# Optimization experiments

Measured on AMD Instinct MI355X. Metric: run time of the kernel, lower is better.

## Reference

```python
import jax, jax.numpy as jnp
import numpy as np

B, NQ, NKV, QD, KVD, AD = 8, 4096, 4096, 1024, 1024, 128

def setup_inputs() -> dict:
    key = jax.random.key(0)
    ks = jax.random.split(key, 6)
    scale = lambda d: 1.0 / np.sqrt(d)
    return {
        "q": jax.random.normal(ks[0], (B, NQ, QD), dtype=jnp.float32),
        "k": jax.random.normal(ks[1], (B, NKV, KVD), dtype=jnp.float32),
        "v": jax.random.normal(ks[2], (B, NKV, KVD), dtype=jnp.float32),
        "Wq": jax.random.normal(ks[3], (QD, AD), dtype=jnp.float32) * scale(QD),
        "Wk": jax.random.normal(ks[4], (KVD, AD), dtype=jnp.float32) * scale(KVD),
        "Wv": jax.random.normal(ks[5], (KVD, AD), dtype=jnp.float32) * scale(KVD),
    }

def reference(q, k, v, Wq, Wk, Wv):
    s = AD ** (-0.5)
    Q = jnp.einsum('bnd,de->bne', q, Wq)   # [B,NQ,AD]
    K = jnp.einsum('bmd,de->bme', k, Wk)   # [B,NKV,AD]
    V = jnp.einsum('bmd,de->bme', v, Wv)   # [B,NKV,AD]
    sc = jnp.einsum('bne,bme->bnm', Q, K) * s  # [B,NQ,NKV]
    att = jax.nn.softmax(sc, axis=-1)
    return jnp.einsum('bnm,bme->bne', att, V)
```

## Files before the change

kernel.cpp:

```cpp
#include <hip/hip_runtime.h>
#include <cstdint>
#include <cstddef>

typedef __bf16 bf16_t;
typedef __bf16 bf16x8 __attribute__((ext_vector_type(8)));
typedef __bf16 bf16x4v __attribute__((ext_vector_type(4)));
typedef float f32x16 __attribute__((ext_vector_type(16)));

static __device__ __forceinline__ f32x16 mfma32(bf16x8 a, bf16x8 b, f32x16 c) {
  return __builtin_amdgcn_mfma_f32_32x32x16_bf16(a, b, c, 0, 0, 0);
}

static __device__ __forceinline__ void gld_lds16(const void* g, void* l) {
  __builtin_amdgcn_global_load_lds(
      (const __attribute__((address_space(1))) unsigned int*)g,
      (__attribute__((address_space(3))) unsigned int*)l, 16, 0, 0);
}

#define CEXP_CONST 0.12754582f


__global__ void wt_kernel(const float* __restrict__ Wq, const float* __restrict__ Wk,
                          const float* __restrict__ Wv, bf16_t* __restrict__ Wt2) {
  int t = blockIdx.x * 256 + threadIdx.x;
  int tensor = t >> 17;
  int r = t & 131071;
  int j = r & 7, l31 = (r >> 3) & 31, h = (r >> 8) & 1, nf = (r >> 9) & 3, k16 = (r >> 11) & 63;
  int k = k16 * 16 + h * 8 + j, n = nf * 32 + l31;
  const float* W = tensor == 0 ? Wq : (tensor == 1 ? Wk : Wv);
  Wt2[t] = (bf16_t)W[(size_t)k * 128 + n];
}

__global__ __launch_bounds__(256, 4) void proj_kernel(
    const float* __restrict__ xq, const float* __restrict__ xk, const float* __restrict__ xv,
    const bf16_t* __restrict__ WtAll,
    bf16_t* __restrict__ Qp, bf16_t* __restrict__ Kp, bf16_t* __restrict__ Vt) {
  __shared__ __align__(16) char smc[16384];
  const int tid = threadIdx.x;
  const int ty = blockIdx.y;
  const int bm = blockIdx.x;
  const float* X = (ty == 0) ? xq : (ty == 1) ? xk : xv;
  const bf16_t* W2 = WtAll + (size_t)ty * 131072;
  const int lane = tid & 63;
  const int w = tid >> 6;
  const int l31 = lane & 31, h = lane >> 5;

  const char* aG = (const char*)X + (size_t)bm * 131072;

  float4 S[4];
  auto ldg = [&](int p) {
#pragma unroll
    for (int i = 0; i < 4; ++i) {
      int c = i * 256 + tid;
      S[i] = *(const float4*)(aG + (size_t)(c >> 5) * 4096 + p * 512 + (c & 31) * 16);
    }
  };
  auto stg = [&](int buf) {
#pragma unroll
    for (int i = 0; i < 4; ++i) {
      int c = i * 256 + tid;
      int row = c >> 5, s = c & 31;
      bf16x4v bv;
      bv[0] = (bf16_t)S[i].x; bv[1] = (bf16_t)S[i].y;
      bv[2] = (bf16_t)S[i].z; bv[3] = (bf16_t)S[i].w;
      int dst = buf * 8192 + row * 256 + ((((s >> 1) ^ (row & 7)) << 4)) + (s & 1) * 8;
      *(uint2*)(smc + dst) = __builtin_bit_cast(uint2, bv);
    }
  };

  bf16x8 wA[8], wB[8];
  const bf16_t* wbase = W2 + w * 512 + lane * 8;
  auto ldw = [&](bf16x8 (&Wf)[8], int p) {
#pragma unroll
    for (int kk = 0; kk < 8; ++kk)
      Wf[kk] = *(const bf16x8*)(wbase + (size_t)(p * 8 + kk) * 2048);
  };

  f32x16 acc;
#pragma unroll
  for (int r = 0; r < 16; ++r) acc[r] = 0.0f;
  const int asw = l31 & 7;
  auto kloop = [&](bf16x8 (&Wf)[8], int buf) {
    const char* arow = smc + buf * 8192 + l31 * 256;
#pragma unroll
    for (int kk = 0; kk < 8; ++kk) {
      bf16x8 af = *(const bf16x8*)(arow + (((kk * 2 + h) ^ asw) << 4));
      acc = mfma32(af, Wf[kk], acc);
    }
  };

  ldg(0);
  stg(0);
  ldg(1);
  ldw(wA, 0);
  __syncthreads();

#pragma unroll
  for (int p2 = 0; p2 < 4; ++p2) {
    const int pe = 2 * p2;
    ldw(wB, pe + 1);
    kloop(wA, 0);
    stg(1);
    if (pe + 2 < 8) ldg(pe + 2);
    __syncthreads();
    const int po = pe + 1;
    if (po + 1 < 8) ldw(wA, po + 1);
    kloop(wB, 1);
    if (po + 1 < 8) {
      stg(0);
      if (po + 2 < 8) ldg(po + 2);
    }
    __syncthreads();
  }

  if (ty < 2) {
    constexpr int RS = 264;
#pragma unroll
    for (int r = 0; r < 16; ++r) {
      int m = (r & 3) + 8 * (r >> 2) + 4 * h;
      *(bf16_t*)(smc + m * RS + (w * 32 + l31) * 2) = (bf16_t)acc[r];
    }
    __syncthreads();
    bf16_t* O = (ty == 0) ? Qp : Kp;
    char* obase = (char*)O + (size_t)bm * 8192;
#pragma unroll
    for (int i = 0; i < 2; ++i) {
      int c = i * 256 + tid;
      int rr = c >> 4, ch = c & 15;
      uint4 vv = *(const uint4*)(smc + rr * RS + ch * 16);
      *(uint4*)(obase + rr * 256 + ch * 16) = vv;
    }
  } else {
#pragma unroll
    for (int q = 0; q < 4; ++q) {
      int n = w * 32 + l31;
      bf16x4v bv;
#pragma unroll
      for (int j = 0; j < 4; ++j) bv[j] = (bf16_t)acc[q * 4 + j];
      *(uint2*)(smc + n * 72 + q * 16 + h * 8) = __builtin_bit_cast(uint2, bv);
    }
    __syncthreads();
    const int bb = bm >> 7;
    const int m0 = (bm & 127) * 32;
    {
      int n = tid >> 1, half = tid & 1;
      const char* src = smc + n * 72 + half * 32;
      char* dst = (char*)Vt + (size_t)bb * 1048576 + (size_t)n * 8192 + m0 * 2 + half * 32;
      uint4 v0 = *(const uint4*)(src);
      uint4 v1 = *(const uint4*)(src + 16);
      *(uint4*)(dst) = v0;
      *(uint4*)(dst + 16) = v1;
    }
  }
}

template <int B0>
static __device__ __forceinline__ bf16x8 build_pf(const f32x16& s, int h) {
  unsigned c0, c1, c2, c3;
  asm("v_cvt_pk_bf16_f32 %0, %1, %2" : "=v"(c0) : "v"(s[B0 + 0]), "v"(s[B0 + 1]));
  asm("v_cvt_pk_bf16_f32 %0, %1, %2" : "=v"(c1) : "v"(s[B0 + 2]), "v"(s[B0 + 3]));
  asm("v_cvt_pk_bf16_f32 %0, %1, %2" : "=v"(c2) : "v"(s[B0 + 4]), "v"(s[B0 + 5]));
  asm("v_cvt_pk_bf16_f32 %0, %1, %2" : "=v"(c3) : "v"(s[B0 + 6]), "v"(s[B0 + 7]));
  unsigned x0 = (unsigned)__shfl_xor((int)c0, 32);
  unsigned x1 = (unsigned)__shfl_xor((int)c1, 32);
  unsigned x2 = (unsigned)__shfl_xor((int)c2, 32);
  unsigned x3 = (unsigned)__shfl_xor((int)c3, 32);
  uint4 u;
  u.x = h ? x2 : c0;
  u.y = h ? x3 : c1;
  u.z = h ? c2 : x0;
  u.w = h ? c3 : x1;
  return __builtin_bit_cast(bf16x8, u);
}

template <int SPLIT>
__global__ __launch_bounds__(256, 2) void attn_kernel(
    const bf16_t* __restrict__ Qp, const bf16_t* __restrict__ Kp,
    const bf16_t* __restrict__ Vt, float* __restrict__ out,
    float* __restrict__ Opart, float* __restrict__ Mpart, float* __restrict__ Lpart) {
  __shared__ __align__(16) char smc[65536];
  const int tid = threadIdx.x;
  const int lane = tid & 63, w = tid >> 6;
  const int l31 = lane & 31, h = lane >> 5;
  const int bid = blockIdx.x;
  const int b = bid & 7;
  const int qt = (bid >> 3) & 31;
  const int s = bid >> 8;
  const int NT = 64 / SPLIT;
  const float CEXP = CEXP_CONST;
  const int qbase = qt * 128 + w * 32;
  const int sw0 = (l31 ^ (l31 >> 3)) & 7;
  const int sw1 = sw0 ^ 4;

  bf16x8 qf[8];
  const bf16_t* qrow = Qp + (size_t)(b * 4096 + qbase + l31) * 128 + h * 8;
#pragma unroll
  for (int db = 0; db < 8; ++db) qf[db] = *(const bf16x8*)(qrow + db * 16);

  int swv[4];
#pragma unroll
  for (int nf = 0; nf < 4; ++nf) swv[nf] = (l31 & 7) ^ ((4 * nf + (l31 >> 3)) & 7);

  const int rl = lane >> 4, slK = lane & 15;
  const int dl = lane >> 3, slV = lane & 7;
  int koff[4], voff[4];
#pragma unroll
  for (int i = 0; i < 4; ++i) {
    int r = w * 16 + i * 4 + rl;
    int swr = (r ^ (r >> 3)) & 7;
    koff[i] = r * 256 + (((slK & 8) | ((slK & 7) ^ swr)) << 4);
    int d = w * 32 + i * 8 + dl;
    int swd = (d ^ (d >> 3)) & 7;
    voff[i] = d * 8192 + ((slV ^ swd) << 4);
  }
  const char* kpb = (const char*)Kp + (size_t)b * 1048576 + (size_t)s * NT * 16384;
  const char* vpb = (const char*)Vt + (size_t)b * 1048576 + (size_t)s * NT * 128;

  f32x16 oacc[4];
#pragma unroll
  for (int nf = 0; nf < 4; ++nf)
#pragma unroll
    for (int r = 0; r < 16; ++r) oacc[nf][r] = 0.0f;
  float m_run = -3.0e38f, lacc = 0.0f;

  auto stage = [&](int tt, int bufb) {
    const char* kb = kpb + (size_t)tt * 16384;
    const char* vb = vpb + (size_t)tt * 128;
    char* lk = smc + bufb + w * 4096;
    char* lv = smc + bufb + 16384 + w * 4096;
#pragma unroll
    for (int i = 0; i < 4; ++i) {
      gld_lds16(kb + koff[i], lk + i * 1024);
      gld_lds16(vb + voff[i], lv + i * 1024);
    }
  };

  stage(0, 0);
  stage(1, 32768);

  for (int t = 0; t < NT; ++t) {
    asm volatile("s_waitcnt vmcnt(8)" ::: "memory");
    __builtin_amdgcn_s_barrier();
    const char* kb = smc + (t & 1) * 32768;
    const char* vb = kb + 16384;

    f32x16 s0, s1;
#pragma unroll
    for (int i = 0; i < 16; ++i) { s0[i] = 0.0f; s1[i] = 0.0f; }
    __builtin_amdgcn_s_setprio(1);
#pragma unroll
    for (int db = 0; db < 8; ++db) {
      const int q = 2 * db + h;
      bf16x8 k0 = *(const bf16x8*)(kb + l31 * 256 + (((q & 8) | ((q & 7) ^ sw0)) << 4));
      bf16x8 k1 = *(const bf16x8*)(kb + (32 + l31) * 256 + (((q & 8) | ((q & 7) ^ sw1)) << 4));
      s0 = mfma32(k0, qf[db], s0);
      s1 = mfma32(k1, qf[db], s1);
    }
    __builtin_amdgcn_s_setprio(0);

    float tmax = fmaxf(s0[0], s1[0]);
#pragma unroll
    for (int i = 1; i < 16; ++i) tmax = fmaxf(tmax, fmaxf(s0[i], s1[i]));
    tmax = fmaxf(tmax, __shfl_xor(tmax, 32));
    if (__any(tmax > m_run + 62.0f)) {
      float mnew = fmaxf(m_run, tmax);
      float fac = exp2f((m_run - mnew) * CEXP);
      m_run = mnew;
      lacc *= fac;
#pragma unroll
      for (int r = 0; r < 16; ++r) {
        float fr = __shfl(fac, (r & 3) + 8 * (r >> 2) + 4 * h);
#pragma unroll
        for (int nf = 0; nf < 4; ++nf) oacc[nf][r] *= fr;
      }
    }
    const float mc = m_run * CEXP;
#pragma unroll
    for (int i = 0; i < 16; ++i) s0[i] = exp2f(fmaf(s0[i], CEXP, -mc));
#pragma unroll
    for (int i = 0; i < 16; ++i) s1[i] = exp2f(fmaf(s1[i], CEXP, -mc));
    float a0 = 0.f, a1 = 0.f, a2 = 0.f, a3 = 0.f;
#pragma unroll
    for (int i = 0; i < 16; i += 4) {
      a0 += s0[i] + s1[i];         a1 += s0[i + 1] + s1[i + 1];
      a2 += s0[i + 2] + s1[i + 2]; a3 += s0[i + 3] + s1[i + 3];
    }
    lacc += (a0 + a1) + (a2 + a3);

    __builtin_amdgcn_s_setprio(1);
    {
      bf16x8 pf = build_pf<0>(s0, h);
#pragma unroll
      for (int nf = 0; nf < 4; ++nf) {
        bf16x8 vf = *(const bf16x8*)(vb + (nf * 32 + l31) * 128 + (((0 + h) ^ swv[nf]) << 4));
        oacc[nf] = mfma32(pf, vf, oacc[nf]);
      }
    }
    {
      bf16x8 pf = build_pf<8>(s0, h);
#pragma unroll
      for (int nf = 0; nf < 4; ++nf) {
        bf16x8 vf = *(const bf16x8*)(vb + (nf * 32 + l31) * 128 + (((2 + h) ^ swv[nf]) << 4));
        oacc[nf] = mfma32(pf, vf, oacc[nf]);
      }
    }
    {
      bf16x8 pf = build_pf<0>(s1, h);
#pragma unroll
      for (int nf = 0; nf < 4; ++nf) {
        bf16x8 vf = *(const bf16x8*)(vb + (nf * 32 + l31) * 128 + (((4 + h) ^ swv[nf]) << 4));
        oacc[nf] = mfma32(pf, vf, oacc[nf]);
      }
    }
    {
      bf16x8 pf = build_pf<8>(s1, h);
#pragma unroll
      for (int nf = 0; nf < 4; ++nf) {
        bf16x8 vf = *(const bf16x8*)(vb + (nf * 32 + l31) * 128 + (((6 + h) ^ swv[nf]) << 4));
        oacc[nf] = mfma32(pf, vf, oacc[nf]);
      }
    }
    __builtin_amdgcn_s_setprio(0);

    __builtin_amdgcn_s_barrier();
    stage((t + 2) & (NT - 1), (t & 1) * 32768);
  }
  asm volatile("s_waitcnt vmcnt(0)" ::: "memory");

  lacc += __shfl_xor(lacc, 32);
  if (SPLIT == 1) {
    const float inv = 1.0f / lacc;
    float* ob = out + (size_t)(b * 4096 + qbase) * 128;
#pragma unroll
    for (int r = 0; r < 16; ++r) {
      const int rowD = (r & 3) + 8 * (r >> 2) + 4 * h;
      float ir = __shfl(inv, rowD);
#pragma unroll
      for (int nf = 0; nf < 4; ++nf)
        ob[(size_t)rowD * 128 + nf * 32 + l31] = oacc[nf][r] * ir;
    }
  } else {
    const int pb = s * 256 + b * 32 + qt;
    if (lane < 32) {
      Mpart[pb * 128 + w * 32 + l31] = m_run;
      Lpart[pb * 128 + w * 32 + l31] = lacc;
    }
    float* ob = Opart + ((size_t)pb * 128 + w * 32) * 128;
#pragma unroll
    for (int r = 0; r < 16; ++r) {
      const int rowD = (r & 3) + 8 * (r >> 2) + 4 * h;
#pragma unroll
      for (int nf = 0; nf < 4; ++nf)
        ob[(size_t)rowD * 128 + nf * 32 + l31] = oacc[nf][r];
    }
  }
}

__global__ __launch_bounds__(256) void combine_kernel(
    const float* __restrict__ Opart, const float* __restrict__ Mpart,
    const float* __restrict__ Lpart, float* __restrict__ out) {
  const int g = blockIdx.x * 8 + (threadIdx.x >> 5);
  const int lane32 = threadIdx.x & 31;
  const int b = g >> 12;
  const int pos = g & 4095;
  const int qt = pos >> 7;
  const int row = pos & 127;
  const int i0 = (b * 32 + qt) * 128 + row;
  const int i1 = (256 + b * 32 + qt) * 128 + row;
  const float m0 = Mpart[i0], m1 = Mpart[i1];
  const float l0 = Lpart[i0], l1 = Lpart[i1];
  const float m = fmaxf(m0, m1);
  const float w0 = exp2f((m0 - m) * CEXP_CONST);
  const float w1 = exp2f((m1 - m) * CEXP_CONST);
  const float inv = 1.0f / (w0 * l0 + w1 * l1);
  const float4 o0 = *(const float4*)(Opart + (size_t)i0 * 128 + lane32 * 4);
  const float4 o1 = *(const float4*)(Opart + (size_t)i1 * 128 + lane32 * 4);
  float4 o;
  o.x = (w0 * o0.x + w1 * o1.x) * inv;
  o.y = (w0 * o0.y + w1 * o1.y) * inv;
  o.z = (w0 * o0.z + w1 * o1.z) * inv;
  o.w = (w0 * o0.w + w1 * o1.w) * inv;
  *(float4*)(out + (size_t)g * 128 + lane32 * 4) = o;
}

extern "C" void kernel_launch(void* const* d_in, const int* in_sizes, int n_in,
                              void* d_out, int out_size, void* d_ws, size_t ws_size,
                              hipStream_t stream) {
  const float* q  = (const float*)d_in[0];
  const float* k  = (const float*)d_in[1];
  const float* v  = (const float*)d_in[2];
  const float* Wq = (const float*)d_in[3];
  const float* Wk = (const float*)d_in[4];
  const float* Wv = (const float*)d_in[5];
  float* out = (float*)d_out;
  char* ws = (char*)d_ws;
  bf16_t* Wt2 = (bf16_t*)(ws);
  bf16_t* Qp = (bf16_t*)(ws + (size_t)(1u << 20));
  bf16_t* Kp = (bf16_t*)(ws + (size_t)(9u << 20));
  bf16_t* Vt = (bf16_t*)(ws + (size_t)(17u << 20));
  float* Opart = (float*)(ws + (size_t)(32u << 20));
  float* Mpart = (float*)(ws + (size_t)(64u << 20));
  float* Lpart = (float*)(ws + (size_t)(64u << 20) + (256u << 10));

  hipLaunchKernelGGL(wt_kernel, dim3(1536), dim3(256), 0, stream, Wq, Wk, Wv, Wt2);
  hipLaunchKernelGGL(proj_kernel, dim3(1024, 3), dim3(256), 0, stream, q, k, v, Wt2, Qp, Kp, Vt);

  if (ws_size >= ((size_t)65 << 20)) {
    hipLaunchKernelGGL((attn_kernel<2>), dim3(512), dim3(256), 0, stream,
                       Qp, Kp, Vt, out, Opart, Mpart, Lpart);
    hipLaunchKernelGGL(combine_kernel, dim3(4096), dim3(256), 0, stream,
                       Opart, Mpart, Lpart, out);
  } else {
    hipLaunchKernelGGL((attn_kernel<1>), dim3(256), dim3(256), 0, stream,
                       Qp, Kp, Vt, out, Opart, Mpart, Lpart);
  }
}
```

Measured before the change: 206.5 us.

## Enlarge projection tile to 64 rows and stage weights through LDS

Each projection block now computes a 64x128 output tile instead of 32x128, with four waves split 2x2 so each wave runs two MFMA accumulators. Weight fragments are staged through double-buffered LDS, where before each wave loaded its own copy from global memory into registers. The K loop runs in 16 smaller steps of 64. The aim is to halve redundant weight traffic per row of X and improve reuse. In exchange it uses 48KB of LDS, lowers the occupancy target from 4 to 3 blocks, and launches half as many blocks.

```diff
diff --git a/kernel.cpp b/kernel.cpp
--- a/kernel.cpp
+++ b/kernel.cpp
@@ -31,11 +31,11 @@
   Wt2[t] = (bf16_t)W[(size_t)k * 128 + n];
 }
 
-__global__ __launch_bounds__(256, 4) void proj_kernel(
+__global__ __launch_bounds__(256, 3) void proj_kernel(
     const float* __restrict__ xq, const float* __restrict__ xk, const float* __restrict__ xv,
     const bf16_t* __restrict__ WtAll,
     bf16_t* __restrict__ Qp, bf16_t* __restrict__ Kp, bf16_t* __restrict__ Vt) {
-  __shared__ __align__(16) char smc[16384];
+  __shared__ __align__(16) char smc[49152];
   const int tid = threadIdx.x;
   const int ty = blockIdx.y;
   const int bm = blockIdx.x;
@@ -44,72 +44,67 @@
   const int lane = tid & 63;
   const int w = tid >> 6;
   const int l31 = lane & 31, h = lane >> 5;
-
-  const char* aG = (const char*)X + (size_t)bm * 131072;
-
-  float4 S[4];
+  const int mh = w & 1, nh = w >> 1;
+
+  const char* aG = (const char*)X + (size_t)bm * 262144;
+  const char* wG = (const char*)W2;
+
+  float4 SX[4];
+  uint4 SW[4];
   auto ldg = [&](int p) {
 #pragma unroll
     for (int i = 0; i < 4; ++i) {
       int c = i * 256 + tid;
-      S[i] = *(const float4*)(aG + (size_t)(c >> 5) * 4096 + p * 512 + (c & 31) * 16);
-    }
+      SX[i] = *(const float4*)(aG + (size_t)(c >> 4) * 4096 + p * 256 + (c & 15) * 16);
+    }
+#pragma unroll
+    for (int i = 0; i < 4; ++i)
+      SW[i] = *(const uint4*)(wG + p * 16384 + (i * 256 + tid) * 16);
   };
   auto stg = [&](int buf) {
 #pragma unroll
     for (int i = 0; i < 4; ++i) {
       int c = i * 256 + tid;
-      int row = c >> 5, s = c & 31;
+      int row = c >> 4, s = c & 15;
       bf16x4v bv;
-      bv[0] = (bf16_t)S[i].x; bv[1] = (bf16_t)S[i].y;
-      bv[2] = (bf16_t)S[i].z; bv[3] = (bf16_t)S[i].w;
-      int dst = buf * 8192 + row * 256 + ((((s >> 1) ^ (row & 7)) << 4)) + (s & 1) * 8;
+      bv[0] = (bf16_t)SX[i].x; bv[1] = (bf16_t)SX[i].y;
+      bv[2] = (bf16_t)SX[i].z; bv[3] = (bf16_t)SX[i].w;
+      int dst = buf * 8192 + row * 128 + (((s >> 1) ^ (row & 7)) << 4) + (s & 1) * 8;
       *(uint2*)(smc + dst) = __builtin_bit_cast(uint2, bv);
     }
+#pragma unroll
+    for (int i = 0; i < 4; ++i)
+      *(uint4*)(smc + 16384 + buf * 16384 + (i * 256 + tid) * 16) = SW[i];
   };
 
-  bf16x8 wA[8], wB[8];
-  const bf16_t* wbase = W2 + w * 512 + lane * 8;
-  auto ldw = [&](bf16x8 (&Wf)[8], int p) {
-#pragma unroll
-    for (int kk = 0; kk < 8; ++kk)
-      Wf[kk] = *(const bf16x8*)(wbase + (size_t)(p * 8 + kk) * 2048);
-  };
-
-  f32x16 acc;
-#pragma unroll
-  for (int r = 0; r < 16; ++r) acc[r] = 0.0f;
+  f32x16 acc0, acc1;
+#pragma unroll
+  for (int r = 0; r < 16; ++r) { acc0[r] = 0.0f; acc1[r] = 0.0f; }
   const int asw = l31 & 7;
-  auto kloop = [&](bf16x8 (&Wf)[8], int buf) {
-    const char* arow = smc + buf * 8192 + l31 * 256;
-#pragma unroll
-    for (int kk = 0; kk < 8; ++kk) {
-      bf16x8 af = *(const bf16x8*)(arow + (((kk * 2 + h) ^ asw) << 4));
-      acc = mfma32(af, Wf[kk], acc);
+
+  auto kloop = [&](int buf) {
+    const char* ab = smc + buf * 8192 + (mh * 32 + l31) * 128;
+    const char* wb = smc + 16384 + buf * 16384 + h * 512 + l31 * 16;
+#pragma unroll
+    for (int k = 0; k < 4; ++k) {
+      bf16x8 af = *(const bf16x8*)(ab + (((2 * k + h) ^ asw) << 4));
+      bf16x8 wf0 = *(const bf16x8*)(wb + (k * 4 + nh * 2 + 0) * 1024);
+      bf16x8 wf1 = *(const bf16x8*)(wb + (k * 4 + nh * 2 + 1) * 1024);
+      acc0 = mfma32(af, wf0, acc0);
+      acc1 = mfma32(af, wf1, acc1);
     }
   };
 
   ldg(0);
   stg(0);
   ldg(1);
-  ldw(wA, 0);
   __syncthreads();
 
-#pragma unroll
-  for (int p2 = 0; p2 < 4; ++p2) {
-    const int pe = 2 * p2;
-    ldw(wB, pe + 1);
-    kloop(wA, 0);
-    stg(1);
-    if (pe + 2 < 8) ldg(pe + 2);
-    __syncthreads();
-    const int po = pe + 1;
-    if (po + 1 < 8) ldw(wA, po + 1);
-    kloop(wB, 1);
-    if (po + 1 < 8) {
-      stg(0);
-      if (po + 2 < 8) ldg(po + 2);
-    }
+#pragma unroll 2
+  for (int p = 0; p < 16; ++p) {
+    kloop(p & 1);
+    if (p + 1 < 16) stg((p + 1) & 1);
+    if (p + 2 < 16) ldg(p + 2);
     __syncthreads();
   }
 
@@ -117,14 +112,15 @@
     constexpr int RS = 264;
 #pragma unroll
     for (int r = 0; r < 16; ++r) {
-      int m = (r & 3) + 8 * (r >> 2) + 4 * h;
-      *(bf16_t*)(smc + m * RS + (w * 32 + l31) * 2) = (bf16_t)acc[r];
+      int m = mh * 32 + (r & 3) + 8 * (r >> 2) + 4 * h;
+      *(bf16_t*)(smc + m * RS + ((nh * 2 + 0) * 32 + l31) * 2) = (bf16_t)acc0[r];
+      *(bf16_t*)(smc + m * RS + ((nh * 2 + 1) * 32 + l31) * 2) = (bf16_t)acc1[r];
     }
     __syncthreads();
     bf16_t* O = (ty == 0) ? Qp : Kp;
-    char* obase = (char*)O + (size_t)bm * 8192;
-#pragma unroll
-    for (int i = 0; i < 2; ++i) {
+    char* obase = (char*)O + (size_t)bm * 16384;
+#pragma unroll
+    for (int i = 0; i < 4; ++i) {
       int c = i * 256 + tid;
       int rr = c >> 4, ch = c & 15;
       uint4 vv = *(const uint4*)(smc + rr * RS + ch * 16);
@@ -132,24 +128,20 @@
     }
   } else {
 #pragma unroll
-    for (int q = 0; q < 4; ++q) {
-      int n = w * 32 + l31;
-      bf16x4v bv;
-#pragma unroll
-      for (int j = 0; j < 4; ++j) bv[j] = (bf16_t)acc[q * 4 + j];
-      *(uint2*)(smc + n * 72 + q * 16 + h * 8) = __builtin_bit_cast(uint2, bv);
+    for (int r = 0; r < 16; ++r) {
+      int m = mh * 32 + (r & 3) + 8 * (r >> 2) + 4 * h;
+      *(bf16_t*)(smc + ((nh * 2 + 0) * 32 + l31) * 136 + m * 2) = (bf16_t)acc0[r];
+      *(bf16_t*)(smc + ((nh * 2 + 1) * 32 + l31) * 136 + m * 2) = (bf16_t)acc1[r];
     }
     __syncthreads();
-    const int bb = bm >> 7;
-    const int m0 = (bm & 127) * 32;
-    {
-      int n = tid >> 1, half = tid & 1;
-      const char* src = smc + n * 72 + half * 32;
-      char* dst = (char*)Vt + (size_t)bb * 1048576 + (size_t)n * 8192 + m0 * 2 + half * 32;
-      uint4 v0 = *(const uint4*)(src);
-      uint4 v1 = *(const uint4*)(src + 16);
-      *(uint4*)(dst) = v0;
-      *(uint4*)(dst + 16) = v1;
+    const int bb = bm >> 6;
+    const int m0b = (bm & 63) * 128;
+#pragma unroll
+    for (int i = 0; i < 4; ++i) {
+      int c = i * 256 + tid;
+      int n = c >> 3, s = c & 7;
+      uint4 vv = *(const uint4*)(smc + n * 136 + s * 16);
+      *(uint4*)((char*)Vt + (size_t)bb * 1048576 + (size_t)n * 8192 + m0b + s * 16) = vv;
     }
   }
 }
@@ -403,7 +395,7 @@
   float* Lpart = (float*)(ws + (size_t)(64u << 20) + (256u << 10));
 
   hipLaunchKernelGGL(wt_kernel, dim3(1536), dim3(256), 0, stream, Wq, Wk, Wv, Wt2);
-  hipLaunchKernelGGL(proj_kernel, dim3(1024, 3), dim3(256), 0, stream, q, k, v, Wt2, Qp, Kp, Vt);
+  hipLaunchKernelGGL(proj_kernel, dim3(512, 3), dim3(256), 0, stream, q, k, v, Wt2, Qp, Kp, Vt);
 
   if (ws_size >= ((size_t)65 << 20)) {
     hipLaunchKernelGGL((attn_kernel<2>), dim3(512), dim3(256), 0, stream,
```

Result: slower. 276.7 us (+34.0%).
